# Performance work log

Measured on AMD Instinct MI355X. Metric: run time of the kernel, lower is better.

## Reference

```python
import jax, jax.numpy as jnp
from jax import lax
import numpy as np

B, H, N, F = 8, 512, 64, 256
P = 12  # prediction_steps


def setup_inputs() -> dict:
    key = jax.random.key(0)
    ks = jax.random.split(key, 6)
    s_in = 1.0 / np.sqrt(N * F)
    s_f = 1.0 / np.sqrt(F)
    return {
        "x": jax.random.normal(ks[0], (B, H, N, F), jnp.float32),
        "W1": jax.random.normal(ks[1], (N * F, F), jnp.float32) * s_in,
        "b1": jnp.zeros((F,), jnp.float32),
        "Wx": jax.random.normal(ks[2], (F, 4 * F), jnp.float32) * s_f,
        "Wh": jax.random.normal(ks[3], (F, 4 * F), jnp.float32) * s_f,
        "b": jnp.zeros((4 * F,), jnp.float32),
        "Wa": jax.random.normal(ks[4], (F, F), jnp.float32) * s_f,
        "ba": jnp.zeros((F,), jnp.float32),
        "W2": jax.random.normal(ks[5], (F, N), jnp.float32) * s_f,
        "b2": jnp.zeros((N,), jnp.float32),
    }


def _lstm_cell(h, c, xt, Wx, Wh, b):
    # Keras LSTMCell gate order: i, f, g(candidate), o
    z = xt @ Wx + h @ Wh + b  # (B, 4F)
    i, f, g, o = jnp.split(z, 4, axis=-1)
    c_new = jax.nn.sigmoid(f) * c + jax.nn.sigmoid(i) * jnp.tanh(g)
    h_new = jax.nn.sigmoid(o) * jnp.tanh(c_new)
    return h_new, c_new


def reference(x, W1, b1, Wx, Wh, b, Wa, ba, W2, b2):
    Bx, Hx, Nx, Fx = x.shape
    xs = x.reshape(Bx, Hx, Nx * Fx) @ W1 + b1  # dense1: (B,H,F)

    def enc_step(carry, xt):
        h, c = carry
        h, c = _lstm_cell(h, c, xt, Wx, Wh, b)
        return (h, c), h

    h0 = jnp.zeros((Bx, Fx), x.dtype)
    (h, c), enc = lax.scan(enc_step, (h0, h0), jnp.swapaxes(xs, 0, 1))
    enc = jnp.swapaxes(enc, 0, 1)  # encoder_states (B,H,F)

    def dec_step(carry, _):
        h, c, mem = carry
        q = mem @ Wa + ba                          # (B,F)
        scores = jnp.einsum('bf,bhf->bh', q, enc)  # dot-product attention
        w = jax.nn.softmax(scores, axis=-1)
        ctx = jnp.einsum('bh,bhf->bf', w, enc)
        h, c = _lstm_cell(h, c, ctx, Wx, Wh, b)
        return (h, c, h), h

    (_, _, _), preds = lax.scan(dec_step, (h, c, h), None, length=P)
    preds = jnp.swapaxes(preds, 0, 1)  # (B,P,F)
    return preds @ W2 + b2  # (B,P,N)
```

## Files before the change

kernel.cpp:

```cpp
#include <hip/hip_runtime.h>
#include <hip/hip_bf16.h>
#include <stdint.h>

#define B_ 8
#define H_ 512
#define F_ 256
#define P_ 12
#define M_ 4096
#define K1_ 16384
#define J_ 1024

typedef __attribute__((ext_vector_type(8))) short short8;
typedef __attribute__((ext_vector_type(4))) float floatx4;

union FragU { uint4 u; short8 s; };

#define OFF_W1H   ((size_t)0)
#define OFF_W1L   ((size_t)8388608)
#define OFF_WHSW  ((size_t)16777216)
#define OFF_ENC   ((size_t)17301504)
#define OFF_C     ((size_t)21495808)
#define OFF_XSUM  ((size_t)21504000)
#define OFF_XPRE  ((size_t)25698304)
#define OFF_P1    ((size_t)42475520)
#define OFF_ENCT  (OFF_P1)
#define OFF_ZG    (OFF_ENCT + (size_t)4194304)

__device__ __forceinline__ unsigned short f2bf(float f) {
  uint32_t u = __float_as_uint(f);
  u += 0x7fffu + ((u >> 16) & 1u);
  return (unsigned short)(u >> 16);
}
__device__ __forceinline__ float bf2f(unsigned short h) {
  return __uint_as_float(((uint32_t)h) << 16);
}
__device__ __forceinline__ float sigm(float x) { return 1.f / (1.f + __expf(-x)); }
__device__ __forceinline__ float tanh_(float x) {
  float ax = fabsf(x);
  float e  = __expf(-2.f * ax);
  float t  = (1.f - e) / (1.f + e);
  return x < 0.f ? -t : t;
}

__global__ void k_prep_w1(const float* __restrict__ W1,
                          uint4* __restrict__ hi, uint4* __restrict__ lo) {
  int idx  = blockIdx.x * 1024 + threadIdx.x;
  int lane = idx & 63;
  int kt   = (idx >> 6) & 511;
  int nt   = idx >> 15;
  int n    = nt * 16 + (lane & 15);
  int kb   = kt * 32 + ((lane >> 4) << 3);
  unsigned short h8[8], l8[8];
#pragma unroll
  for (int j = 0; j < 8; ++j) {
    float v = W1[(size_t)(kb + j) * 256 + n];
    unsigned short hh = f2bf(v);
    h8[j] = hh;
    l8[j] = f2bf(v - bf2f(hh));
  }
  uint4 uh, ul;
  uh.x = (uint32_t)h8[0] | ((uint32_t)h8[1] << 16);
  uh.y = (uint32_t)h8[2] | ((uint32_t)h8[3] << 16);
  uh.z = (uint32_t)h8[4] | ((uint32_t)h8[5] << 16);
  uh.w = (uint32_t)h8[6] | ((uint32_t)h8[7] << 16);
  ul.x = (uint32_t)l8[0] | ((uint32_t)l8[1] << 16);
  ul.y = (uint32_t)l8[2] | ((uint32_t)l8[3] << 16);
  ul.z = (uint32_t)l8[4] | ((uint32_t)l8[5] << 16);
  ul.w = (uint32_t)l8[6] | ((uint32_t)l8[7] << 16);
  hi[idx] = uh;
  lo[idx] = ul;
}

__global__ void k_prep_wh(const float* __restrict__ Wh, uint4* __restrict__ sw) {
  int idx  = blockIdx.x * 1024 + threadIdx.x;
  int lane = idx & 63;
  int kt   = (idx >> 6) & 7;
  int zt   = idx >> 9;
  int col  = zt * 16 + (lane & 15);
  int kb   = kt * 32 + ((lane >> 4) << 3);
  unsigned short h8[8];
#pragma unroll
  for (int j = 0; j < 8; ++j) h8[j] = f2bf(Wh[(size_t)(kb + j) * 1024 + col]);
  uint4 u;
  u.x = (uint32_t)h8[0] | ((uint32_t)h8[1] << 16);
  u.y = (uint32_t)h8[2] | ((uint32_t)h8[3] << 16);
  u.z = (uint32_t)h8[4] | ((uint32_t)h8[5] << 16);
  u.w = (uint32_t)h8[6] | ((uint32_t)h8[7] << 16);
  sw[idx] = u;
}

__global__ __launch_bounds__(1024)
void k_gemm1(const float* __restrict__ x, const uint4* __restrict__ w1h,
             const uint4* __restrict__ w1l, float* __restrict__ P1) {
  __shared__ __align__(16) unsigned short xh[128 * 40];
  __shared__ __align__(16) unsigned short xl[128 * 40];
  int bm = blockIdx.x >> 3, kc = blockIdx.x & 7;
  int m0 = bm * 128, kcbase = kc * 2048;
  int tid = threadIdx.x, wave = tid >> 6, lane = tid & 63;
  int quad = lane >> 4, l15 = lane & 15;
  int srow = tid >> 3, skch = tid & 7;
  floatx4 acc[8];
#pragma unroll
  for (int mt = 0; mt < 8; ++mt) acc[mt] = (floatx4)(0.f);

  const float* xrow = x + (size_t)(m0 + srow) * K1_ + kcbase + skch * 4;
  float4 xv = *(const float4*)(xrow);
  for (int it = 0; it < 64; ++it) {
    unsigned short h0 = f2bf(xv.x), h1 = f2bf(xv.y), h2 = f2bf(xv.z), h3 = f2bf(xv.w);
    unsigned short g0 = f2bf(xv.x - bf2f(h0)), g1 = f2bf(xv.y - bf2f(h1));
    unsigned short g2 = f2bf(xv.z - bf2f(h2)), g3 = f2bf(xv.w - bf2f(h3));
    uint2 ph, pl;
    ph.x = (uint32_t)h0 | ((uint32_t)h1 << 16); ph.y = (uint32_t)h2 | ((uint32_t)h3 << 16);
    pl.x = (uint32_t)g0 | ((uint32_t)g1 << 16); pl.y = (uint32_t)g2 | ((uint32_t)g3 << 16);
    *(uint2*)&xh[srow * 40 + skch * 4] = ph;
    *(uint2*)&xl[srow * 40 + skch * 4] = pl;
    __syncthreads();

    float4 xn = xv;
    if (it < 63) xn = *(const float4*)(xrow + (it + 1) * 32);

    size_t aoff = (size_t)(wave * 512 + kc * 64 + it) * 64 + lane;
    FragU ah; ah.u = w1h[aoff];
    FragU al; al.u = w1l[aoff];
#pragma unroll
    for (int mt = 0; mt < 8; ++mt) {
      FragU bh, bl;
      bh.u = *(const uint4*)&xh[(mt * 16 + l15) * 40 + quad * 8];
      bl.u = *(const uint4*)&xl[(mt * 16 + l15) * 40 + quad * 8];
      acc[mt] = __builtin_amdgcn_mfma_f32_16x16x32_bf16(ah.s, bh.s, acc[mt], 0, 0, 0);
      acc[mt] = __builtin_amdgcn_mfma_f32_16x16x32_bf16(ah.s, bl.s, acc[mt], 0, 0, 0);
      acc[mt] = __builtin_amdgcn_mfma_f32_16x16x32_bf16(al.s, bh.s, acc[mt], 0, 0, 0);
    }
    __syncthreads();
    xv = xn;
  }
  int nbase = wave * 16 + quad * 4;
#pragma unroll
  for (int mt = 0; mt < 8; ++mt) {
    int m = m0 + mt * 16 + l15;
#pragma unroll
    for (int r = 0; r < 4; ++r)
      P1[(size_t)(kc * 256 + nbase + r) * M_ + m] = acc[mt][r];
  }
}

__global__ void k_reduce(const float* __restrict__ P1, const float* __restrict__ b1,
                         float* __restrict__ xsum) {
  int idx = blockIdx.x * 1024 + threadIdx.x;
  int k = idx >> 12, m = idx & 4095;
  float s = b1[k];
#pragma unroll
  for (int kc = 0; kc < 8; ++kc) s += P1[(size_t)(kc * 256 + k) * M_ + m];
  xsum[(size_t)k * M_ + m] = s;
}

__global__ __launch_bounds__(256)
void k_gemm2(const float* __restrict__ xsum, const float* __restrict__ Wx,
             const float* __restrict__ bz, float* __restrict__ Xpre) {
  int m0 = blockIdx.x * 16;
  int j = threadIdx.x;
  float acc0[16], acc1[16], acc2[16], acc3[16];
  float bb0 = bz[j], bb1 = bz[256 + j], bb2 = bz[512 + j], bb3 = bz[768 + j];
#pragma unroll
  for (int mm = 0; mm < 16; ++mm) { acc0[mm] = bb0; acc1[mm] = bb1; acc2[mm] = bb2; acc3[mm] = bb3; }
#pragma unroll 4
  for (int k = 0; k < 256; ++k) {
    float w0 = Wx[(size_t)k * 1024 + j];
    float w1 = Wx[(size_t)k * 1024 + 256 + j];
    float w2 = Wx[(size_t)k * 1024 + 512 + j];
    float w3 = Wx[(size_t)k * 1024 + 768 + j];
#pragma unroll
    for (int mm = 0; mm < 16; ++mm) {
      float xv = xsum[(size_t)k * M_ + m0 + mm];
      acc0[mm] += xv * w0; acc1[mm] += xv * w1; acc2[mm] += xv * w2; acc3[mm] += xv * w3;
    }
  }
#pragma unroll
  for (int mm = 0; mm < 16; ++mm) {
    float* o = Xpre + (size_t)(m0 + mm) * 1024;
    o[j] = acc0[mm]; o[256 + j] = acc1[mm]; o[512 + j] = acc2[mm]; o[768 + j] = acc3[mm];
  }
}

__global__ __attribute__((amdgpu_flat_work_group_size(512, 512)))
__attribute__((amdgpu_waves_per_eu(2, 2)))
void k_encoder(const uint4* __restrict__ whsw, const float* __restrict__ Xpre,
               float* __restrict__ enc, float* __restrict__ encT,
               float* __restrict__ cws) {
  __shared__ uint4 wl[9216];
  __shared__ __align__(16) unsigned short hb[2][512];
  __shared__ __align__(16) float zsh[2048];
  int b = blockIdx.x, tid = threadIdx.x;
  int wave = tid >> 6, lane = tid & 63;
  int quad = lane >> 4, l15 = lane & 15;
  int e = tid & 1, j = tid >> 1;

  for (int r = 0; r < 18; ++r) {
    int u = r * 512 + tid;
    int ln = u & 63, fslot = u >> 6;
    int w = fslot / 18, fi = fslot - w * 18;
    int i = (fi < 8) ? 6 : ((fi < 16) ? 7 : 5);
    int kt = (fi < 8) ? fi : ((fi < 16) ? fi - 8 : fi - 10);
    int zt = 16 * (i >> 1) + 2 * w + (i & 1);
    wl[u] = whsw[(size_t)((zt * 8 + kt) * 64 + ln)];
  }

  uint4 wfr[46];
#pragma unroll
  for (int i = 0; i < 5; ++i) {
    int zt = 16 * (i >> 1) + 2 * wave + (i & 1);
#pragma unroll
    for (int kt = 0; kt < 8; ++kt)
      wfr[i * 8 + kt] = whsw[(size_t)((zt * 8 + kt) * 64 + lane)];
  }
  {
    int zt = 33 + 2 * wave;
#pragma unroll
    for (int kt = 0; kt < 6; ++kt)
      wfr[40 + kt] = whsw[(size_t)((zt * 8 + kt) * 64 + lane)];
  }

  hb[0][tid] = 0; hb[1][tid] = 0;
  float c_ = 0.f;
  const float* xpb = Xpre + (size_t)b * 512 * 1024;
  int colA = 256 * e + j;
  int colB = 512 + colA;
  int hoff  = ((l15 == 1) ? 256 : 0) + quad * 8;
  int zwoff = ((l15 == 1) ? 1024 : 0) + quad * 4;
  const uint4* wlw = wl + (size_t)(wave * 18) * 64 + lane;
  __syncthreads();

  int cur = 0;
  for (int t = 0; t < 512; ++t) {
    const unsigned short* hbc = hb[cur];
    float xA = xpb[(size_t)t * 1024 + colA];
    float xB = xpb[(size_t)t * 1024 + colB];

    {
      floatx4 a0 = (floatx4)(0.f), a1 = (floatx4)(0.f);
      floatx4 a2 = (floatx4)(0.f), a3 = (floatx4)(0.f);
      FragU bf; bf.u = *(const uint4*)&hbc[hoff];
#pragma unroll
      for (int kt = 0; kt < 8; ++kt) {
        FragU bfn;
        if (kt < 7) bfn.u = *(const uint4*)&hbc[hoff + (kt + 1) * 32];
        FragU f0, f1, f2, f3;
        f0.u = wfr[0 + kt];  f1.u = wfr[8 + kt];
        f2.u = wfr[16 + kt]; f3.u = wfr[24 + kt];
        a0 = __builtin_amdgcn_mfma_f32_16x16x32_bf16(f0.s, bf.s, a0, 0, 0, 0);
        a1 = __builtin_amdgcn_mfma_f32_16x16x32_bf16(f1.s, bf.s, a1, 0, 0, 0);
        a2 = __builtin_amdgcn_mfma_f32_16x16x32_bf16(f2.s, bf.s, a2, 0, 0, 0);
        a3 = __builtin_amdgcn_mfma_f32_16x16x32_bf16(f3.s, bf.s, a3, 0, 0, 0);
        if (kt < 7) bf = bfn;
      }
      if (l15 < 2) {
        *(floatx4*)&zsh[zwoff + (2 * wave) * 16]      = a0;
        *(floatx4*)&zsh[zwoff + (2 * wave + 1) * 16]  = a1;
        *(floatx4*)&zsh[zwoff + (16 + 2 * wave) * 16] = a2;
        *(floatx4*)&zsh[zwoff + (17 + 2 * wave) * 16] = a3;
      }
    }
    {
      floatx4 a4 = (floatx4)(0.f), a5 = (floatx4)(0.f);
      floatx4 a6 = (floatx4)(0.f), a7 = (floatx4)(0.f);
      FragU p5a, p5b;
      p5a.u = wlw[(size_t)16 * 64];
      p5b.u = wlw[(size_t)17 * 64];
      FragU bf, p6, p7;
      bf.u = *(const uint4*)&hbc[hoff];
      p6.u = wlw[0];
      p7.u = wlw[(size_t)8 * 64];
#pragma unroll
      for (int kt = 0; kt < 8; ++kt) {
        FragU bfn, p6n, p7n;
        if (kt < 7) {
          bfn.u = *(const uint4*)&hbc[hoff + (kt + 1) * 32];
          p6n.u = wlw[(size_t)(kt + 1) * 64];
          p7n.u = wlw[(size_t)(9 + kt) * 64];
        }
        FragU f4; f4.u = wfr[32 + kt];
        a4 = __builtin_amdgcn_mfma_f32_16x16x32_bf16(f4.s, bf.s, a4, 0, 0, 0);
        if (kt < 6) {
          FragU f5; f5.u = wfr[40 + kt];
          a5 = __builtin_amdgcn_mfma_f32_16x16x32_bf16(f5.s, bf.s, a5, 0, 0, 0);
        } else if (kt == 6) {
          a5 = __builtin_amdgcn_mfma_f32_16x16x32_bf16(p5a.s, bf.s, a5, 0, 0, 0);
        } else {
          a5 = __builtin_amdgcn_mfma_f32_16x16x32_bf16(p5b.s, bf.s, a5, 0, 0, 0);
        }
        a6 = __builtin_amdgcn_mfma_f32_16x16x32_bf16(p6.s, bf.s, a6, 0, 0, 0);
        a7 = __builtin_amdgcn_mfma_f32_16x16x32_bf16(p7.s, bf.s, a7, 0, 0, 0);
        if (kt < 7) { bf = bfn; p6 = p6n; p7 = p7n; }
      }
      if (l15 < 2) {
        *(floatx4*)&zsh[zwoff + (32 + 2 * wave) * 16] = a4;
        *(floatx4*)&zsh[zwoff + (33 + 2 * wave) * 16] = a5;
        *(floatx4*)&zsh[zwoff + (48 + 2 * wave) * 16] = a6;
        *(floatx4*)&zsh[zwoff + (49 + 2 * wave) * 16] = a7;
      }
    }

    float zA = zsh[colA] + zsh[1024 + colA] + xA;
    float zB = zsh[colB] + zsh[1024 + colB] + xB;
    float actA = sigm(zA);
    float tnh = tanh_(zB), sg = sigm(zB);
    float actB = e ? sg : tnh;
    float p = actA * actB;
    float send = e ? actA : p;
    float recv = __shfl_xor(send, 1, 64);
    float cn = e ? (actA * c_ + recv)
                 : (recv * c_ + p);
    c_ = cn;
    float th = tanh_(cn);
    float hn = actB * th;
    int nxt = cur ^ 1;
    if (e) {
      enc[((size_t)b * 512 + t) * 256 + j] = hn;
      encT[((size_t)b * 256 + j) * 512 + t] = hn;
      unsigned short hh = f2bf(hn);
      hb[nxt][j] = hh;
      hb[nxt][256 + j] = f2bf(hn - bf2f(hh));
    }
    __syncthreads();
    cur = nxt;
  }
  if (e) cws[b * 256 + j] = c_;
}

__global__ __launch_bounds__(1024)
void k_dec_step(const float* __restrict__ enc, const float* __restrict__ encT,
                float* __restrict__ cst, float* __restrict__ zg,
                const float* __restrict__ Wx, const float* __restrict__ Wh,
                const float* __restrict__ bz,
                const float* __restrict__ Wa, const float* __restrict__ ba,
                const float* __restrict__ W2, const float* __restrict__ b2,
                float* __restrict__ out, int p) {
  __shared__ float hsh[256], qsh[256], ctxs[256], sc[512], smx[2];
  __shared__ float zb[1024];
  int b = blockIdx.x, tid = threadIdx.x;
  const float* encb = enc + (size_t)b * 512 * 256;

  if (p > 0) {
    if (tid < 256) {
      float zi = zg[b * 1024 + tid];
      float zf = zg[b * 1024 + 256 + tid];
      float zgg = zg[b * 1024 + 512 + tid];
      float zo = zg[b * 1024 + 768 + tid];
      float ig = sigm(zi), fg = sigm(zf), gg = tanh_(zgg), og = sigm(zo);
      float cn = fg * cst[b * 256 + tid] + ig * gg;
      cst[b * 256 + tid] = cn;
      hsh[tid] = og * tanh_(cn);
    }
    __syncthreads();
    if (tid < 512) {
      int col = tid & 63, kc = tid >> 6;
      float s = 0.f;
#pragma unroll
      for (int i = 0; i < 32; ++i) {
        int k = kc * 32 + i;
        s += hsh[k] * W2[(size_t)k * 64 + col];
      }
      zb[tid] = s;
    }
    __syncthreads();
    if (tid < 64) {
      float s = b2[tid];
#pragma unroll
      for (int kc = 0; kc < 8; ++kc) s += zb[kc * 64 + tid];
      out[((size_t)b * 12 + (p - 1)) * 64 + tid] = s;
    }
  } else {
    if (tid < 256) hsh[tid] = encb[(size_t)511 * 256 + tid];
  }
  if (p == 12) return;
  __syncthreads();

  {
    int jj = tid & 255, kc = tid >> 8;
    float s = 0.f;
#pragma unroll 8
    for (int i = 0; i < 64; ++i) {
      int k = kc * 64 + i;
      s += hsh[k] * Wa[(size_t)k * 256 + jj];
    }
    zb[tid] = s;
  }
  __syncthreads();
  if (tid < 256) qsh[tid] = ba[tid] + zb[tid] + zb[256 + tid] + zb[512 + tid] + zb[768 + tid];
  __syncthreads();

  {
    int hh = tid & 511, kc = tid >> 9;
    const float* eT = encT + (size_t)b * 256 * 512;
    float s = 0.f;
#pragma unroll 8
    for (int i = 0; i < 128; ++i) {
      int k = kc * 128 + i;
      s += qsh[k] * eT[(size_t)k * 512 + hh];
    }
    zb[tid] = s;
  }
  __syncthreads();
  if (tid < 512) sc[tid] = zb[tid] + zb[512 + tid];
  __syncthreads();

  if (tid < 64) {
    float m = -3.4e38f;
#pragma unroll
    for (int r = 0; r < 8; ++r) m = fmaxf(m, sc[tid * 8 + r]);
#pragma unroll
    for (int off = 32; off >= 1; off >>= 1) m = fmaxf(m, __shfl_xor(m, off, 64));
    if (tid == 0) smx[0] = m;
  }
  __syncthreads();
  if (tid < 512) sc[tid] = __expf(sc[tid] - smx[0]);
  __syncthreads();
  if (tid < 64) {
    float s = 0.f;
#pragma unroll
    for (int r = 0; r < 8; ++r) s += sc[tid * 8 + r];
#pragma unroll
    for (int off = 32; off >= 1; off >>= 1) s += __shfl_xor(s, off, 64);
    if (tid == 0) smx[1] = 1.f / s;
  }
  __syncthreads();

  {
    int jj = tid & 255, hs = tid >> 8;
    float s = 0.f;
#pragma unroll 8
    for (int r = 0; r < 128; ++r) {
      int hh = hs * 128 + r;
      s += sc[hh] * encb[(size_t)hh * 256 + jj];
    }
    zb[tid] = s;
  }
  __syncthreads();
  if (tid < 256)
    ctxs[tid] = (zb[tid] + zb[256 + tid] + zb[512 + tid] + zb[768 + tid]) * smx[1];
  __syncthreads();

  {
    float s = bz[tid];
#pragma unroll 16
    for (int k = 0; k < 256; ++k)
      s += ctxs[k] * Wx[(size_t)k * 1024 + tid] + hsh[k] * Wh[(size_t)k * 1024 + tid];
    zg[b * 1024 + tid] = s;
  }
}

extern "C" void kernel_launch(void* const* d_in, const int* in_sizes, int n_in,
                              void* d_out, int out_size, void* d_ws, size_t ws_size,
                              hipStream_t stream) {
  const float* x  = (const float*)d_in[0];
  const float* W1 = (const float*)d_in[1];
  const float* b1 = (const float*)d_in[2];
  const float* Wx = (const float*)d_in[3];
  const float* Wh = (const float*)d_in[4];
  const float* bz = (const float*)d_in[5];
  const float* Wa = (const float*)d_in[6];
  const float* ba = (const float*)d_in[7];
  const float* W2 = (const float*)d_in[8];
  const float* b2 = (const float*)d_in[9];

  char* ws = (char*)d_ws;
  uint4* w1h  = (uint4*)(ws + OFF_W1H);
  uint4* w1l  = (uint4*)(ws + OFF_W1L);
  uint4* whsw = (uint4*)(ws + OFF_WHSW);
  float* enc  = (float*)(ws + OFF_ENC);
  float* cws  = (float*)(ws + OFF_C);
  float* xsum = (float*)(ws + OFF_XSUM);
  float* xpre = (float*)(ws + OFF_XPRE);
  float* p1   = (float*)(ws + OFF_P1);
  float* encT = (float*)(ws + OFF_ENCT);
  float* zg   = (float*)(ws + OFF_ZG);

  k_prep_w1<<<dim3(512), dim3(1024), 0, stream>>>(W1, w1h, w1l);
  k_prep_wh<<<dim3(32), dim3(1024), 0, stream>>>(Wh, whsw);
  k_gemm1<<<dim3(256), dim3(1024), 0, stream>>>(x, w1h, w1l, p1);
  k_reduce<<<dim3(1024), dim3(1024), 0, stream>>>(p1, b1, xsum);
  k_gemm2<<<dim3(256), dim3(256), 0, stream>>>(xsum, Wx, bz, xpre);
  k_encoder<<<dim3(8), dim3(512), 0, stream>>>(whsw, xpre, enc, encT, cws);
  for (int p = 0; p <= 12; ++p)
    k_dec_step<<<dim3(8), dim3(1024), 0, stream>>>(enc, encT, cws, zg,
                                                   Wx, Wh, bz, Wa, ba, W2, b2,
                                                   (float*)d_out, p);
}
```

Before: 1.942 ms.

## Split decoder step across 8 blocks per batch with double-buffered gate state

Result: slower. 2.076 ms (+6.9%).

```diff
diff --git a/kernel.cpp b/kernel.cpp
--- a/kernel.cpp
+++ b/kernel.cpp
@@ -25,6 +25,7 @@
 #define OFF_P1    ((size_t)42475520)
 #define OFF_ENCT  (OFF_P1)
 #define OFF_ZG    (OFF_ENCT + (size_t)4194304)
+#define OFF_CB    (OFF_ZG + (size_t)65536)
 
 __device__ __forceinline__ unsigned short f2bf(float f) {
   uint32_t u = __float_as_uint(f);
@@ -327,32 +328,48 @@
   if (e) cws[b * 256 + j] = c_;
 }
 
-__global__ __launch_bounds__(1024)
-void k_dec_step(const float* __restrict__ enc, const float* __restrict__ encT,
-                float* __restrict__ cst, float* __restrict__ zg,
-                const float* __restrict__ Wx, const float* __restrict__ Wh,
-                const float* __restrict__ bz,
-                const float* __restrict__ Wa, const float* __restrict__ ba,
-                const float* __restrict__ W2, const float* __restrict__ b2,
-                float* __restrict__ out, int p) {
-  __shared__ float hsh[256], qsh[256], ctxs[256], sc[512], smx[2];
-  __shared__ float zb[1024];
-  int b = blockIdx.x, tid = threadIdx.x;
+__global__ __launch_bounds__(512)
+void k_dec_m(const float* __restrict__ enc, const float* __restrict__ encT,
+             const float* __restrict__ cws,
+             const float* __restrict__ Wx, const float* __restrict__ Wh,
+             const float* __restrict__ bz, const float* __restrict__ Wa,
+             const float* __restrict__ ba, const float* __restrict__ W2,
+             const float* __restrict__ b2, float* __restrict__ zg,
+             float* __restrict__ cbuf, float* __restrict__ out, int p) {
+  __shared__ float hsh[256], csh[256], qsh[256], ctxf[256];
+  __shared__ float wsh[512], red[512];
+  __shared__ float sred[16];
+  __shared__ float sinv;
+  int blk = blockIdx.x;
+  int b = blk >> 3, sub = blk & 7;
+  int tid = threadIdx.x;
   const float* encb = enc + (size_t)b * 512 * 256;
-
-  if (p > 0) {
+  const float* eTb  = encT + (size_t)b * 256 * 512;
+
+  if (p == 0) {
     if (tid < 256) {
-      float zi = zg[b * 1024 + tid];
-      float zf = zg[b * 1024 + 256 + tid];
-      float zgg = zg[b * 1024 + 512 + tid];
-      float zo = zg[b * 1024 + 768 + tid];
+      hsh[tid] = encb[(size_t)511 * 256 + tid];
+      csh[tid] = cws[b * 256 + tid];
+    }
+  } else {
+    const float* zp = zg + (size_t)((p + 1) & 1) * 8192 + b * 1024;
+    const float* cp = cbuf + (size_t)((p + 1) & 1) * 2048 + b * 256;
+    if (tid < 256) {
+      float zi = zp[tid];
+      float zf = zp[256 + tid];
+      float zgg = zp[512 + tid];
+      float zo = zp[768 + tid];
       float ig = sigm(zi), fg = sigm(zf), gg = tanh_(zgg), og = sigm(zo);
-      float cn = fg * cst[b * 256 + tid] + ig * gg;
-      cst[b * 256 + tid] = cn;
+      float cn = fg * cp[tid] + ig * gg;
+      csh[tid] = cn;
       hsh[tid] = og * tanh_(cn);
     }
-    __syncthreads();
-    if (tid < 512) {
+  }
+  __syncthreads();
+
+  if (sub == 0) {
+    if (tid < 256) cbuf[(size_t)(p & 1) * 2048 + b * 256 + tid] = csh[tid];
+    if (p > 0) {
       int col = tid & 63, kc = tid >> 6;
       float s = 0.f;
 #pragma unroll
@@ -360,92 +377,96 @@
         int k = kc * 32 + i;
         s += hsh[k] * W2[(size_t)k * 64 + col];
       }
-      zb[tid] = s;
-    }
-    __syncthreads();
-    if (tid < 64) {
-      float s = b2[tid];
-#pragma unroll
-      for (int kc = 0; kc < 8; ++kc) s += zb[kc * 64 + tid];
-      out[((size_t)b * 12 + (p - 1)) * 64 + tid] = s;
-    }
-  } else {
-    if (tid < 256) hsh[tid] = encb[(size_t)511 * 256 + tid];
+      red[tid] = s;
+      __syncthreads();
+      if (tid < 64) {
+        float t = b2[tid];
+#pragma unroll
+        for (int kc2 = 0; kc2 < 8; ++kc2) t += red[kc2 * 64 + tid];
+        out[((size_t)b * 12 + (p - 1)) * 64 + tid] = t;
+      }
+      __syncthreads();
+    }
   }
   if (p == 12) return;
-  __syncthreads();
 
   {
-    int jj = tid & 255, kc = tid >> 8;
+    int j = tid & 255, half = tid >> 8;
+    float s = 0.f;
+#pragma unroll 8
+    for (int i = 0; i < 128; ++i) {
+      int k = half * 128 + i;
+      s += hsh[k] * Wa[(size_t)k * 256 + j];
+    }
+    red[tid] = s;
+  }
+  __syncthreads();
+  if (tid < 256) qsh[tid] = ba[tid] + red[tid] + red[256 + tid];
+  __syncthreads();
+
+  float sv = 0.f;
+#pragma unroll 8
+  for (int k = 0; k < 256; ++k)
+    sv += qsh[k] * eTb[(size_t)k * 512 + tid];
+
+  {
+    float m = sv;
+#pragma unroll
+    for (int off = 32; off >= 1; off >>= 1) m = fmaxf(m, __shfl_xor(m, off, 64));
+    if ((tid & 63) == 0) sred[tid >> 6] = m;
+    __syncthreads();
+    if (tid == 0) {
+      float mm = sred[0];
+#pragma unroll
+      for (int i2 = 1; i2 < 8; ++i2) mm = fmaxf(mm, sred[i2]);
+      sred[8] = mm;
+    }
+    __syncthreads();
+    float e = __expf(sv - sred[8]);
+    wsh[tid] = e;
+    float s2 = e;
+#pragma unroll
+    for (int off = 32; off >= 1; off >>= 1) s2 += __shfl_xor(s2, off, 64);
+    if ((tid & 63) == 0) sred[tid >> 6] = s2;
+    __syncthreads();
+    if (tid == 0) {
+      float ss = 0.f;
+#pragma unroll
+      for (int i2 = 0; i2 < 8; ++i2) ss += sred[i2];
+      sinv = 1.f / ss;
+    }
+    __syncthreads();
+  }
+
+  {
+    int j = tid & 255, half = tid >> 8;
+    float s = 0.f;
+#pragma unroll 8
+    for (int r = 0; r < 256; ++r) {
+      int hh = half * 256 + r;
+      s += wsh[hh] * encb[(size_t)hh * 256 + j];
+    }
+    red[tid] = s;
+  }
+  __syncthreads();
+  if (tid < 256) ctxf[tid] = (red[tid] + red[256 + tid]) * sinv;
+  __syncthreads();
+
+  {
+    int col = sub * 128 + (tid & 127), ks = tid >> 7;
     float s = 0.f;
 #pragma unroll 8
     for (int i = 0; i < 64; ++i) {
-      int k = kc * 64 + i;
-      s += hsh[k] * Wa[(size_t)k * 256 + jj];
-    }
-    zb[tid] = s;
-  }
-  __syncthreads();
-  if (tid < 256) qsh[tid] = ba[tid] + zb[tid] + zb[256 + tid] + zb[512 + tid] + zb[768 + tid];
-  __syncthreads();
-
-  {
-    int hh = tid & 511, kc = tid >> 9;
-    const float* eT = encT + (size_t)b * 256 * 512;
-    float s = 0.f;
-#pragma unroll 8
-    for (int i = 0; i < 128; ++i) {
-      int k = kc * 128 + i;
-      s += qsh[k] * eT[(size_t)k * 512 + hh];
-    }
-    zb[tid] = s;
-  }
-  __syncthreads();
-  if (tid < 512) sc[tid] = zb[tid] + zb[512 + tid];
-  __syncthreads();
-
-  if (tid < 64) {
-    float m = -3.4e38f;
-#pragma unroll
-    for (int r = 0; r < 8; ++r) m = fmaxf(m, sc[tid * 8 + r]);
-#pragma unroll
-    for (int off = 32; off >= 1; off >>= 1) m = fmaxf(m, __shfl_xor(m, off, 64));
-    if (tid == 0) smx[0] = m;
-  }
-  __syncthreads();
-  if (tid < 512) sc[tid] = __expf(sc[tid] - smx[0]);
-  __syncthreads();
-  if (tid < 64) {
-    float s = 0.f;
-#pragma unroll
-    for (int r = 0; r < 8; ++r) s += sc[tid * 8 + r];
-#pragma unroll
-    for (int off = 32; off >= 1; off >>= 1) s += __shfl_xor(s, off, 64);
-    if (tid == 0) smx[1] = 1.f / s;
-  }
-  __syncthreads();
-
-  {
-    int jj = tid & 255, hs = tid >> 8;
-    float s = 0.f;
-#pragma unroll 8
-    for (int r = 0; r < 128; ++r) {
-      int hh = hs * 128 + r;
-      s += sc[hh] * encb[(size_t)hh * 256 + jj];
-    }
-    zb[tid] = s;
-  }
-  __syncthreads();
-  if (tid < 256)
-    ctxs[tid] = (zb[tid] + zb[256 + tid] + zb[512 + tid] + zb[768 + tid]) * smx[1];
-  __syncthreads();
-
-  {
-    float s = bz[tid];
-#pragma unroll 16
-    for (int k = 0; k < 256; ++k)
-      s += ctxs[k] * Wx[(size_t)k * 1024 + tid] + hsh[k] * Wh[(size_t)k * 1024 + tid];
-    zg[b * 1024 + tid] = s;
+      int k = ks * 64 + i;
+      s += ctxf[k] * Wx[(size_t)k * 1024 + col] + hsh[k] * Wh[(size_t)k * 1024 + col];
+    }
+    red[tid] = s;
+  }
+  __syncthreads();
+  if (tid < 128) {
+    int col = sub * 128 + tid;
+    zg[(size_t)(p & 1) * 8192 + b * 1024 + col] =
+        bz[col] + red[tid] + red[128 + tid] + red[256 + tid] + red[384 + tid];
   }
 }
 
@@ -474,6 +495,7 @@
   float* p1   = (float*)(ws + OFF_P1);
   float* encT = (float*)(ws + OFF_ENCT);
   float* zg   = (float*)(ws + OFF_ZG);
+  float* cbuf = (float*)(ws + OFF_CB);
 
   k_prep_w1<<<dim3(512), dim3(1024), 0, stream>>>(W1, w1h, w1l);
   k_prep_wh<<<dim3(32), dim3(1024), 0, stream>>>(Wh, whsw);
@@ -482,7 +504,7 @@
   k_gemm2<<<dim3(256), dim3(256), 0, stream>>>(xsum, Wx, bz, xpre);
   k_encoder<<<dim3(8), dim3(512), 0, stream>>>(whsw, xpre, enc, encT, cws);
   for (int p = 0; p <= 12; ++p)
-    k_dec_step<<<dim3(8), dim3(1024), 0, stream>>>(enc, encT, cws, zg,
-                                                   Wx, Wh, bz, Wa, ba, W2, b2,
-                                                   (float*)d_out, p);
-}
+    k_dec_m<<<dim3(64), dim3(512), 0, stream>>>(enc, encT, cws, Wx, Wh, bz,
+                                                Wa, ba, W2, b2, zg, cbuf,
+                                                (float*)d_out, p);
+}
```
